# Kernel optimization log

Measured on AMD Instinct MI355X. Metric: run time of the kernel, lower is better.

The kernel has to match this reference:

```python
import jax, jax.numpy as jnp
import numpy as np

V, D, H, L, B = 30000, 128, 4, 128, 512
HD = D // H  # head dim = 32
NL = 2       # num xLSTM layers


def _layernorm(x, w, b):
    mu = x.mean(-1, keepdims=True)
    var = x.var(-1, keepdims=True)
    return (x - mu) * jax.lax.rsqrt(var + 1e-5) * w + b


def _groupnorm_heads(h, w):
    # GroupNorm with num_groups = H over the channel dim (per-head norm), h: [B,L,D]
    hh = h.reshape(h.shape[0], h.shape[1], H, HD)
    mu = hh.mean(-1, keepdims=True)
    var = hh.var(-1, keepdims=True)
    hh = (hh - mu) * jax.lax.rsqrt(var + 1e-5)
    return hh.reshape(h.shape) * w


def _slstm_block(x, W, R, b, gnw, lnw, lnb):
    # x: [B,L,D]; W: [4,D,D] input gate projections (i,f,z,o); R: [4,H,HD,HD] block-diagonal
    # per-head recurrent weights; b: [4,D]; gnw: [D] groupnorm scale.
    bsz = x.shape[0]
    xn = _layernorm(x, lnw, lnb)
    pre = jnp.einsum('bld,god->lbgo', xn, W) + b  # [L,B,4,D]

    def step(carry, pre_t):
        h, c, n, m = carry  # each [B,D]
        rec = jnp.einsum('bhd,ghde->bghe', h.reshape(bsz, H, HD), R).reshape(bsz, 4, D)
        g = pre_t + rec
        it, ft, zt, ot = g[:, 0], g[:, 1], g[:, 2], g[:, 3]
        # stabilized exponential gating (sLSTM vanilla backend)
        m_new = jnp.maximum(ft + m, it)
        i = jnp.exp(it - m_new)
        f = jnp.exp(ft + m - m_new)
        c_new = f * c + i * jnp.tanh(zt)
        n_new = f * n + i
        h_new = jax.nn.sigmoid(ot) * c_new / n_new
        return (h_new, c_new, n_new, m_new), h_new

    z = jnp.zeros((bsz, D), x.dtype)
    _, hs = jax.lax.scan(step, (z, z, z, z), pre)
    hs = jnp.transpose(hs, (1, 0, 2))  # [B,L,D]
    return x + _groupnorm_heads(hs, gnw)  # residual block


def setup_inputs() -> dict:
    key = jax.random.key(0)
    ks = jax.random.split(key, 10)
    s = lambda k, shape, sc: jax.random.normal(k, shape, jnp.float32) * sc
    return {
        'x_ids': jax.random.randint(ks[0], (B, L), 0, V),
        'emb': s(ks[1], (V, D), 0.02),
        'ln_w': jnp.ones((NL, D), jnp.float32),
        'ln_b': jnp.zeros((NL, D), jnp.float32),
        'Wg': s(ks[2], (NL, 4, D, D), 0.05),
        'Rg': s(ks[3], (NL, 4, H, HD, HD), 0.05),
        'bg': s(ks[4], (NL, 4, D), 0.02),
        'gn_w': jnp.ones((NL, D), jnp.float32),
        'w1': s(ks[5], (64, D), 0.05),
        'b1': jnp.zeros((64,), jnp.float32),
        'w2': s(ks[6], (2, 64), 0.05),
        'b2': jnp.zeros((2,), jnp.float32),
    }


def reference(x_ids, emb, ln_w, ln_b, Wg, Rg, bg, gn_w, w1, b1, w2, b2):
    x = emb[x_ids]  # [B,L,D] embedding lookup
    for l in range(NL):
        x = _slstm_block(x, Wg[l], Rg[l], bg[l], gn_w[l], ln_w[l], ln_b[l])
    pooled = x.mean(axis=1)  # mean over sequence, [B,D]
    hid = jax.nn.relu(pooled @ w1.T + b1)  # dropout is identity at eval
    return hid @ w2.T + b2  # [B,2] logits
```

## Files before the change

### kernel.cpp

```cpp
#include <hip/hip_runtime.h>

typedef _Float16 f16;
typedef unsigned int uint;
typedef f16 f16x2 __attribute__((ext_vector_type(2)));
typedef f16 f16x8 __attribute__((ext_vector_type(8)));
typedef __fp16 h16x2 __attribute__((ext_vector_type(2)));
typedef float f32x4 __attribute__((ext_vector_type(4)));

#define Bn 512
#define Ln 128
#define Dn 128
#define Cn 512

__device__ __forceinline__ float fdot2f(uint a, uint b, float c) {
#if __has_builtin(__builtin_amdgcn_fdot2)
  return __builtin_amdgcn_fdot2(__builtin_bit_cast(f16x2, a),
                                __builtin_bit_cast(f16x2, b), c, false);
#else
  f16x2 av = __builtin_bit_cast(f16x2, a), bv = __builtin_bit_cast(f16x2, b);
  return c + (float)av[0] * (float)bv[0] + (float)av[1] * (float)bv[1];
#endif
}

__device__ __forceinline__ uint pk2(float a, float b) {
#if __has_builtin(__builtin_amdgcn_cvt_pkrtz)
  h16x2 v = __builtin_amdgcn_cvt_pkrtz(a, b);
  return __builtin_bit_cast(uint, v);
#else
  f16x2 v; v[0] = (f16)a; v[1] = (f16)b;
  return __builtin_bit_cast(uint, v);
#endif
}

template<int CTRL>
__device__ __forceinline__ float rorf(float x) {
#if __has_builtin(__builtin_amdgcn_mov_dpp)
  int r = __builtin_amdgcn_mov_dpp(__builtin_bit_cast(int, x), CTRL, 0xF, 0xF, true);
  return __builtin_bit_cast(float, r);
#else
  return __shfl_xor(x, (CTRL - 0x120));
#endif
}

__device__ __forceinline__ int swz16i(float x) {
#if __has_builtin(__builtin_amdgcn_ds_swizzle)
  return __builtin_amdgcn_ds_swizzle(__builtin_bit_cast(int, x), 0x401F);
#else
  return __builtin_bit_cast(int, __shfl_xor(x, 16));
#endif
}

__device__ __forceinline__ void read_hu(const f16* base, uint hu[16]) {
  const uint4* hq = (const uint4*)base;
  uint4 q0 = hq[0], q1 = hq[1], q2 = hq[2], q3 = hq[3];
  hu[0]=q0.x; hu[1]=q0.y; hu[2]=q0.z; hu[3]=q0.w;
  hu[4]=q1.x; hu[5]=q1.y; hu[6]=q1.z; hu[7]=q1.w;
  hu[8]=q2.x; hu[9]=q2.y; hu[10]=q2.z; hu[11]=q2.w;
  hu[12]=q3.x; hu[13]=q3.y; hu[14]=q3.z; hu[15]=q3.w;
}

__global__ __launch_bounds__(256) void k_embed_ln(const int* __restrict__ ids,
                                                  const float* __restrict__ emb,
                                                  const float* __restrict__ lw,
                                                  const float* __restrict__ lb,
                                                  float* __restrict__ x,
                                                  f16* __restrict__ xn) {
  int row = blockIdx.x * 4 + (threadIdx.x >> 6);
  int lane = threadIdx.x & 63;
  int id = ids[row];
  const float* er = emb + (size_t)id * Dn;
  float a = er[lane], b = er[lane + 64];
  float s1 = a + b, s2 = a * a + b * b;
  #pragma unroll
  for (int off = 32; off; off >>= 1) {
    s1 += __shfl_xor(s1, off);
    s2 += __shfl_xor(s2, off);
  }
  float mu = s1 * (1.f / 128.f);
  float var = s2 * (1.f / 128.f) - mu * mu;
  float rs = rsqrtf(var + 1e-5f);
  float* xr = x + (size_t)row * Dn;
  xr[lane] = a; xr[lane + 64] = b;
  f16* xo = xn + (size_t)row * Dn;
  xo[lane]      = (f16)((a - mu) * rs * lw[lane] + lb[lane]);
  xo[lane + 64] = (f16)((b - mu) * rs * lw[lane + 64] + lb[lane + 64]);
}

__global__ __launch_bounds__(256) void k_convert(const float* __restrict__ Wg,
                                                 const float* __restrict__ Rg,
                                                 f16* __restrict__ WhF,
                                                 f16* __restrict__ RT) {
  int i = blockIdx.x * 256 + threadIdx.x;
  const int nWfrag = 2 * 4 * 32 * 64;
  if (i < nWfrag) {
    int lane = i & 63;
    int ii   = (i >> 6) & 31;
    int kk   = (i >> 11) & 3;
    int l    = i >> 13;
    int c = ii * 16 + (lane & 15);
    int d = kk * 32 + ((lane >> 4) << 3);
    const float* src = Wg + ((size_t)(l * 512 + c) * 128 + d);
    f16* dst = WhF + (size_t)i * 8;
    #pragma unroll
    for (int j = 0; j < 8; ++j) dst[j] = (f16)src[j];
  } else {
    int j = i - nWfrag;
    if (j < 32768) {
      int dd = j & 31;
      int e  = (j >> 5) & 31;
      int hh = (j >> 10) & 3;
      int g  = (j >> 12) & 3;
      int l  = j >> 14;
      RT[j] = (f16)Rg[((((l * 4 + g) * 4 + hh) * 32 + dd) * 32) + e];
    }
  }
}

__global__ __launch_bounds__(256) void k_ln(const float* __restrict__ x,
                                            const float* __restrict__ lw,
                                            const float* __restrict__ lb,
                                            f16* __restrict__ xn) {
  int row = blockIdx.x * 4 + (threadIdx.x >> 6);
  int lane = threadIdx.x & 63;
  const float* xr = x + (size_t)row * Dn;
  float a = xr[lane], b = xr[lane + 64];
  float s1 = a + b, s2 = a * a + b * b;
  #pragma unroll
  for (int off = 32; off; off >>= 1) {
    s1 += __shfl_xor(s1, off);
    s2 += __shfl_xor(s2, off);
  }
  float mu = s1 * (1.f / 128.f);
  float var = s2 * (1.f / 128.f) - mu * mu;
  float rs = rsqrtf(var + 1e-5f);
  f16* xo = xn + (size_t)row * Dn;
  xo[lane]      = (f16)((a - mu) * rs * lw[lane] + lb[lane]);
  xo[lane + 64] = (f16)((b - mu) * rs * lw[lane + 64] + lb[lane + 64]);
}

__global__ __launch_bounds__(256) void k_gemm(const f16* __restrict__ xn,
                                              const f16* __restrict__ WhF,
                                              const float* __restrict__ bias,
                                              uint2* __restrict__ preP) {
  int w = threadIdx.x >> 6;
  int lane = threadIdx.x & 63;
  int l16 = lane & 15, quad = lane >> 4;
  int m0 = blockIdx.x * 64 + w * 16;

  float bv[32];
  #pragma unroll
  for (int i = 0; i < 32; ++i) bv[i] = bias[i * 16 + l16];

  f16x8 a[4];
  const f16* arow = xn + (size_t)(m0 + l16) * Dn + quad * 8;
  #pragma unroll
  for (int kk = 0; kk < 4; ++kk) a[kk] = *(const f16x8*)(arow + kk * 32);

  f32x4 acc[32] = {};
  const f16* bbase = WhF + (size_t)lane * 8;
  #pragma unroll
  for (int kk = 0; kk < 4; ++kk) {
    #pragma unroll
    for (int i = 0; i < 32; ++i) {
      f16x8 bf = *(const f16x8*)(bbase + (size_t)(kk * 32 + i) * 512);
      acc[i] = __builtin_amdgcn_mfma_f32_16x16x32_f16(a[kk], bf, acc[i], 0, 0, 0);
    }
  }
  #pragma unroll
  for (int r = 0; r < 4; ++r) {
    int m = m0 + quad * 4 + r;
    #pragma unroll
    for (int i7 = 0; i7 < 8; ++i7) {
      uint2 v;
      v.x = pk2(acc[i7][r]      + bv[i7],      acc[i7 + 8][r]  + bv[i7 + 8]);
      v.y = pk2(acc[i7 + 16][r] + bv[i7 + 16], acc[i7 + 24][r] + bv[i7 + 24]);
      preP[(size_t)m * Dn + i7 * 16 + l16] = v;
    }
  }
}

template<int LAST>
__global__ __launch_bounds__(256, 1) void k_scan(const uint2* __restrict__ preP,
                                                 const f16* __restrict__ RT,
                                                 const float* __restrict__ gnw,
                                                 const float* __restrict__ xin,
                                                 float* __restrict__ xout,
                                                 float* __restrict__ pooled) {
  const int w = threadIdx.x >> 6;
  const int lane = threadIdx.x & 63;
  const int s = w >> 1;
  const int b = blockIdx.x * 2 + s;
  const int d = ((w & 1) << 6) + lane;
  const int head = d >> 5;
  const int e = d & 31;
  const int half = lane >> 5;

  __shared__ __align__(16) f16 hsh[4][64];

  uint rr[4][16];
  const uint* RT32 = (const uint*)RT;
  #pragma unroll
  for (int g = 0; g < 4; ++g) {
    const uint* p = RT32 + ((g * 4 + head) * 32 + e) * 16;
    #pragma unroll
    for (int j = 0; j < 16; ++j) rr[g][j] = p[j];
  }
  const float gw = gnw[d];
  const f16* hbase = &hsh[w][half * 32];

  hsh[w][lane] = (f16)0.f;

  const uint2* pp = preP + (size_t)b * Ln * Dn + d;
  const float* xp = xin + (size_t)b * Ln * Dn + d;
  float* xo = xout + (size_t)b * Ln * Dn + d;

  uint2 pb[4]; float xb[4];
  #pragma unroll
  for (int k = 0; k < 4; ++k) { pb[k] = pp[(size_t)k * Dn]; xb[k] = xp[(size_t)k * Dn]; }

  uint hu[16];
  read_hu(hbase, hu);

  float cc = 0.f, nc = 0.f, mc = 0.f, psum = 0.f;
  float hprev = 0.f, xprev = 0.f;
  float u1 = 0.f, u2 = 0.f;
  int   w1 = 0,   w2 = 0;

  #pragma unroll 1
  for (int t = 0; t < Ln; t += 4) {
    #pragma unroll
    for (int k = 0; k < 4; ++k) {
      int tt = t + k;
      uint2 pc = pb[k]; float xc = xb[k];
      pb[k] = pp[(size_t)(tt + 4) * Dn];
      xb[k] = xp[(size_t)(tt + 4) * Dn];

      if (tt > 0) {
        float s1 = u1 + __builtin_bit_cast(float, w1);
        float s2 = u2 + __builtin_bit_cast(float, w2);
        float mu = s1 * (1.f / 32.f);
        float va = s2 * (1.f / 32.f) - mu * mu;
        float ov = xprev + (hprev - mu) * rsqrtf(va + 1e-5f) * gw;
        if (LAST) psum += ov;
        else      xo[(size_t)(tt - 1) * Dn] = ov;
      }

      float a0 = 0.f, a1 = 0.f, a2 = 0.f, a3 = 0.f;
      float c0 = 0.f, c1 = 0.f, c2 = 0.f, c3 = 0.f;
      #pragma unroll
      for (int j = 0; j < 8; ++j) {
        a0 = fdot2f(hu[j], rr[0][j], a0);
        a1 = fdot2f(hu[j], rr[1][j], a1);
        a2 = fdot2f(hu[j], rr[2][j], a2);
        a3 = fdot2f(hu[j], rr[3][j], a3);
        c0 = fdot2f(hu[j + 8], rr[0][j + 8], c0);
        c1 = fdot2f(hu[j + 8], rr[1][j + 8], c1);
        c2 = fdot2f(hu[j + 8], rr[2][j + 8], c2);
        c3 = fdot2f(hu[j + 8], rr[3][j + 8], c3);
      }
      f16x2 lo = __builtin_bit_cast(f16x2, pc.x);
      f16x2 hi = __builtin_bit_cast(f16x2, pc.y);
      float it = ((float)lo[0] + a0) + c0;
      float ft = ((float)lo[1] + a1) + c1;
      float zt = ((float)hi[0] + a2) + c2;
      float ot = ((float)hi[1] + a3) + c3;

      float mn = fmaxf(ft + mc, it);
      float iv = __expf(it - mn);
      float fv = __expf(ft + mc - mn);
      float zc = fminf(fmaxf(zt, -15.f), 15.f);
      float ez = __expf(2.f * zc);
      float tz = (ez - 1.f) * __builtin_amdgcn_rcpf(ez + 1.f);
      float cn = fv * cc + iv * tz;
      float nn = fv * nc + iv;
      float hn = cn * __builtin_amdgcn_rcpf((1.f + __expf(-ot)) * nn);
      cc = cn; nc = nn; mc = mn;

      hsh[w][lane] = (f16)hn;

      float t1v = hn, t2v = hn * hn;
      t1v += rorf<0x121>(t1v);  t2v += rorf<0x121>(t2v);
      t1v += rorf<0x122>(t1v);  t2v += rorf<0x122>(t2v);
      t1v += rorf<0x124>(t1v);  t2v += rorf<0x124>(t2v);
      t1v += rorf<0x128>(t1v);  t2v += rorf<0x128>(t2v);
      w1 = swz16i(t1v);
      w2 = swz16i(t2v);
      u1 = t1v; u2 = t2v;

      read_hu(hbase, hu);

      hprev = hn; xprev = xc;
    }
  }

  {
    float s1 = u1 + __builtin_bit_cast(float, w1);
    float s2 = u2 + __builtin_bit_cast(float, w2);
    float mu = s1 * (1.f / 32.f);
    float va = s2 * (1.f / 32.f) - mu * mu;
    float ov = xprev + (hprev - mu) * rsqrtf(va + 1e-5f) * gw;
    if (LAST) {
      psum += ov;
      pooled[b * Dn + d] = psum * (1.f / 128.f);
    } else {
      xo[(size_t)(Ln - 1) * Dn] = ov;
    }
  }
}

__global__ __launch_bounds__(64) void k_head(const float* __restrict__ pooled,
                                             const float* __restrict__ w1,
                                             const float* __restrict__ b1,
                                             const float* __restrict__ w2,
                                             const float* __restrict__ b2,
                                             float* __restrict__ out) {
  int b = blockIdx.x;
  int tid = threadIdx.x;
  __shared__ float pool[128];
  __shared__ float hid[64];
  pool[tid]      = pooled[b * Dn + tid];
  pool[tid + 64] = pooled[b * Dn + tid + 64];
  __syncthreads();
  {
    float a = b1[tid];
    const float* wr = w1 + (size_t)tid * Dn;
    #pragma unroll 4
    for (int dd = 0; dd < Dn; ++dd) a += pool[dd] * wr[dd];
    hid[tid] = fmaxf(a, 0.f);
  }
  __syncthreads();
  if (tid < 2) {
    float a = b2[tid];
    const float* wr = w2 + tid * 64;
    #pragma unroll 4
    for (int j = 0; j < 64; ++j) a += hid[j] * wr[j];
    out[b * 2 + tid] = a;
  }
}

extern "C" void kernel_launch(void* const* d_in, const int* in_sizes, int n_in,
                              void* d_out, int out_size, void* d_ws, size_t ws_size,
                              hipStream_t stream) {
  const int*   ids  = (const int*)d_in[0];
  const float* emb  = (const float*)d_in[1];
  const float* ln_w = (const float*)d_in[2];
  const float* ln_b = (const float*)d_in[3];
  const float* Wg   = (const float*)d_in[4];
  const float* Rg   = (const float*)d_in[5];
  const float* bg   = (const float*)d_in[6];
  const float* gn_w = (const float*)d_in[7];
  const float* w1   = (const float*)d_in[8];
  const float* b1   = (const float*)d_in[9];
  const float* w2   = (const float*)d_in[10];
  const float* b2   = (const float*)d_in[11];
  float* out = (float*)d_out;

  char* ws = (char*)d_ws;
  float* x     = (float*)ws;
  f16*   xn    = (f16*)(ws + 33554432);
  uint2* preP  = (uint2*)(ws + 33554432 + 16777216);
  f16*   WhF   = (f16*)(ws + 117440512);
  f16*   RT    = (f16*)(ws + 117440512 + 262144);
  float* pooled= (float*)(ws + 117440512 + 262144 + 65536);

  k_embed_ln<<<16384, 256, 0, stream>>>(ids, emb, ln_w, ln_b, x, xn);
  k_convert<<<192, 256, 0, stream>>>(Wg, Rg, WhF, RT);

  k_gemm<<<1024, 256, 0, stream>>>(xn, WhF, bg, preP);
  k_scan<0><<<256, 256, 0, stream>>>(preP, RT, gn_w, x, x, nullptr);
  k_ln<<<16384, 256, 0, stream>>>(x, ln_w + Dn, ln_b + Dn, xn);
  k_gemm<<<1024, 256, 0, stream>>>(xn, WhF + 65536, bg + Cn, preP);
  k_scan<1><<<256, 256, 0, stream>>>(preP, RT + 16384, gn_w + Dn, x, nullptr, pooled);

  k_head<<<512, 64, 0, stream>>>(pooled, w1, b1, w2, b2, out);
}
```

Baseline: 266.8 us.

## Fuse embedding gather and layernorm into GEMM, fold head into final scan

Measured after the change: 269.9 us. About the same (+1.2%).

```diff
diff --git a/kernel.cpp b/kernel.cpp
--- a/kernel.cpp
+++ b/kernel.cpp
@@ -57,33 +57,6 @@
   hu[4]=q1.x; hu[5]=q1.y; hu[6]=q1.z; hu[7]=q1.w;
   hu[8]=q2.x; hu[9]=q2.y; hu[10]=q2.z; hu[11]=q2.w;
   hu[12]=q3.x; hu[13]=q3.y; hu[14]=q3.z; hu[15]=q3.w;
-}
-
-__global__ __launch_bounds__(256) void k_embed_ln(const int* __restrict__ ids,
-                                                  const float* __restrict__ emb,
-                                                  const float* __restrict__ lw,
-                                                  const float* __restrict__ lb,
-                                                  float* __restrict__ x,
-                                                  f16* __restrict__ xn) {
-  int row = blockIdx.x * 4 + (threadIdx.x >> 6);
-  int lane = threadIdx.x & 63;
-  int id = ids[row];
-  const float* er = emb + (size_t)id * Dn;
-  float a = er[lane], b = er[lane + 64];
-  float s1 = a + b, s2 = a * a + b * b;
-  #pragma unroll
-  for (int off = 32; off; off >>= 1) {
-    s1 += __shfl_xor(s1, off);
-    s2 += __shfl_xor(s2, off);
-  }
-  float mu = s1 * (1.f / 128.f);
-  float var = s2 * (1.f / 128.f) - mu * mu;
-  float rs = rsqrtf(var + 1e-5f);
-  float* xr = x + (size_t)row * Dn;
-  xr[lane] = a; xr[lane + 64] = b;
-  f16* xo = xn + (size_t)row * Dn;
-  xo[lane]      = (f16)((a - mu) * rs * lw[lane] + lb[lane]);
-  xo[lane + 64] = (f16)((b - mu) * rs * lw[lane + 64] + lb[lane + 64]);
 }
 
 __global__ __launch_bounds__(256) void k_convert(const float* __restrict__ Wg,
@@ -116,29 +89,11 @@
   }
 }
 
-__global__ __launch_bounds__(256) void k_ln(const float* __restrict__ x,
-                                            const float* __restrict__ lw,
-                                            const float* __restrict__ lb,
-                                            f16* __restrict__ xn) {
-  int row = blockIdx.x * 4 + (threadIdx.x >> 6);
-  int lane = threadIdx.x & 63;
-  const float* xr = x + (size_t)row * Dn;
-  float a = xr[lane], b = xr[lane + 64];
-  float s1 = a + b, s2 = a * a + b * b;
-  #pragma unroll
-  for (int off = 32; off; off >>= 1) {
-    s1 += __shfl_xor(s1, off);
-    s2 += __shfl_xor(s2, off);
-  }
-  float mu = s1 * (1.f / 128.f);
-  float var = s2 * (1.f / 128.f) - mu * mu;
-  float rs = rsqrtf(var + 1e-5f);
-  f16* xo = xn + (size_t)row * Dn;
-  xo[lane]      = (f16)((a - mu) * rs * lw[lane] + lb[lane]);
-  xo[lane + 64] = (f16)((b - mu) * rs * lw[lane + 64] + lb[lane + 64]);
-}
-
-__global__ __launch_bounds__(256) void k_gemm(const f16* __restrict__ xn,
+template<int EMB>
+__global__ __launch_bounds__(256) void k_gemm(const float* __restrict__ xsrc,
+                                              const int* __restrict__ ids,
+                                              const float* __restrict__ lw,
+                                              const float* __restrict__ lb,
                                               const f16* __restrict__ WhF,
                                               const float* __restrict__ bias,
                                               uint2* __restrict__ preP) {
@@ -147,14 +102,50 @@
   int l16 = lane & 15, quad = lane >> 4;
   int m0 = blockIdx.x * 64 + w * 16;
 
+  const float* src;
+  if (EMB) src = xsrc + (size_t)ids[m0 + l16] * Dn;
+  else     src = xsrc + (size_t)(m0 + l16) * Dn;
+  const float* sp = src + quad * 8;
+
+  f32x4 v[4][2];
+  #pragma unroll
+  for (int kk = 0; kk < 4; ++kk) {
+    v[kk][0] = *(const f32x4*)(sp + kk * 32);
+    v[kk][1] = *(const f32x4*)(sp + kk * 32 + 4);
+  }
+  float s1 = 0.f, s2 = 0.f;
+  #pragma unroll
+  for (int kk = 0; kk < 4; ++kk)
+    #pragma unroll
+    for (int p = 0; p < 2; ++p)
+      #pragma unroll
+      for (int j = 0; j < 4; ++j) {
+        float vv = v[kk][p][j];
+        s1 += vv; s2 = fmaf(vv, vv, s2);
+      }
+  s1 += __shfl_xor(s1, 16);  s2 += __shfl_xor(s2, 16);
+  s1 += __shfl_xor(s1, 32);  s2 += __shfl_xor(s2, 32);
+  float mu = s1 * (1.f / 128.f);
+  float var = s2 * (1.f / 128.f) - mu * mu;
+  float rs = rsqrtf(var + 1e-5f);
+
+  f16x8 a[4];
+  #pragma unroll
+  for (int kk = 0; kk < 4; ++kk) {
+    #pragma unroll
+    for (int p = 0; p < 2; ++p) {
+      int d0 = kk * 32 + quad * 8 + p * 4;
+      f32x4 lw4 = *(const f32x4*)(lw + d0);
+      f32x4 lb4 = *(const f32x4*)(lb + d0);
+      #pragma unroll
+      for (int j = 0; j < 4; ++j)
+        a[kk][p * 4 + j] = (f16)((v[kk][p][j] - mu) * rs * lw4[j] + lb4[j]);
+    }
+  }
+
   float bv[32];
   #pragma unroll
   for (int i = 0; i < 32; ++i) bv[i] = bias[i * 16 + l16];
-
-  f16x8 a[4];
-  const f16* arow = xn + (size_t)(m0 + l16) * Dn + quad * 8;
-  #pragma unroll
-  for (int kk = 0; kk < 4; ++kk) a[kk] = *(const f16x8*)(arow + kk * 32);
 
   f32x4 acc[32] = {};
   const f16* bbase = WhF + (size_t)lane * 8;
@@ -171,10 +162,10 @@
     int m = m0 + quad * 4 + r;
     #pragma unroll
     for (int i7 = 0; i7 < 8; ++i7) {
-      uint2 v;
-      v.x = pk2(acc[i7][r]      + bv[i7],      acc[i7 + 8][r]  + bv[i7 + 8]);
-      v.y = pk2(acc[i7 + 16][r] + bv[i7 + 16], acc[i7 + 24][r] + bv[i7 + 24]);
-      preP[(size_t)m * Dn + i7 * 16 + l16] = v;
+      uint2 vv;
+      vv.x = pk2(acc[i7][r]      + bv[i7],      acc[i7 + 8][r]  + bv[i7 + 8]);
+      vv.y = pk2(acc[i7 + 16][r] + bv[i7 + 16], acc[i7 + 24][r] + bv[i7 + 24]);
+      preP[(size_t)m * Dn + i7 * 16 + l16] = vv;
     }
   }
 }
@@ -183,9 +174,14 @@
 __global__ __launch_bounds__(256, 1) void k_scan(const uint2* __restrict__ preP,
                                                  const f16* __restrict__ RT,
                                                  const float* __restrict__ gnw,
-                                                 const float* __restrict__ xin,
+                                                 const float* __restrict__ xsrc,
+                                                 const int* __restrict__ ids,
                                                  float* __restrict__ xout,
-                                                 float* __restrict__ pooled) {
+                                                 const float* __restrict__ hw1,
+                                                 const float* __restrict__ hb1,
+                                                 const float* __restrict__ hw2,
+                                                 const float* __restrict__ hb2,
+                                                 float* __restrict__ out) {
   const int w = threadIdx.x >> 6;
   const int lane = threadIdx.x & 63;
   const int s = w >> 1;
@@ -196,6 +192,8 @@
   const int half = lane >> 5;
 
   __shared__ __align__(16) f16 hsh[4][64];
+  __shared__ float pool2[2][128];
+  __shared__ float hid2[2][64];
 
   uint rr[4][16];
   const uint* RT32 = (const uint*)RT;
@@ -211,12 +209,21 @@
   hsh[w][lane] = (f16)0.f;
 
   const uint2* pp = preP + (size_t)b * Ln * Dn + d;
-  const float* xp = xin + (size_t)b * Ln * Dn + d;
+  const float* xp = xsrc + (size_t)b * Ln * Dn + d;
+  const int*   idr = ids + b * Ln;
   float* xo = xout + (size_t)b * Ln * Dn + d;
 
-  uint2 pb[4]; float xb[4];
-  #pragma unroll
-  for (int k = 0; k < 4; ++k) { pb[k] = pp[(size_t)k * Dn]; xb[k] = xp[(size_t)k * Dn]; }
+  uint2 pb[4]; float xb[4]; int idb[4];
+  #pragma unroll
+  for (int k = 0; k < 4; ++k) {
+    pb[k] = pp[(size_t)k * Dn];
+    if (LAST) {
+      xb[k] = xp[(size_t)k * Dn];
+    } else {
+      xb[k] = xsrc[(size_t)idr[k] * Dn + d];
+      idb[k] = idr[k + 4];
+    }
+  }
 
   uint hu[16];
   read_hu(hbase, hu);
@@ -233,7 +240,13 @@
       int tt = t + k;
       uint2 pc = pb[k]; float xc = xb[k];
       pb[k] = pp[(size_t)(tt + 4) * Dn];
-      xb[k] = xp[(size_t)(tt + 4) * Dn];
+      if (LAST) {
+        xb[k] = xp[(size_t)(tt + 4) * Dn];
+      } else {
+        xb[k] = xsrc[(size_t)idb[k] * Dn + d];
+        int ni = tt + 8;
+        idb[k] = idr[ni > 127 ? 127 : ni];
+      }
 
       if (tt > 0) {
         float s1 = u1 + __builtin_bit_cast(float, w1);
@@ -301,40 +314,32 @@
     float ov = xprev + (hprev - mu) * rsqrtf(va + 1e-5f) * gw;
     if (LAST) {
       psum += ov;
-      pooled[b * Dn + d] = psum * (1.f / 128.f);
+      pool2[s][d] = psum * (1.f / 128.f);
+      __syncthreads();
+      if ((w & 1) == 0) {
+        int sq = w >> 1;
+        float acc = hb1[lane];
+        const float* wr = hw1 + (size_t)lane * Dn;
+        const float* pl = &pool2[sq][0];
+        #pragma unroll 8
+        for (int dd = 0; dd < Dn; dd += 4) {
+          f32x4 wv = *(const f32x4*)(wr + dd);
+          acc += wv[0]*pl[dd] + wv[1]*pl[dd+1] + wv[2]*pl[dd+2] + wv[3]*pl[dd+3];
+        }
+        hid2[sq][lane] = fmaxf(acc, 0.f);
+      }
+      __syncthreads();
+      if ((w & 1) == 0 && lane < 2) {
+        int sq = w >> 1;
+        float acc = hb2[lane];
+        const float* wr = hw2 + lane * 64;
+        #pragma unroll 4
+        for (int j = 0; j < 64; ++j) acc += hid2[sq][j] * wr[j];
+        out[(blockIdx.x * 2 + sq) * 2 + lane] = acc;
+      }
     } else {
       xo[(size_t)(Ln - 1) * Dn] = ov;
     }
-  }
-}
-
-__global__ __launch_bounds__(64) void k_head(const float* __restrict__ pooled,
-                                             const float* __restrict__ w1,
-                                             const float* __restrict__ b1,
-                                             const float* __restrict__ w2,
-                                             const float* __restrict__ b2,
-                                             float* __restrict__ out) {
-  int b = blockIdx.x;
-  int tid = threadIdx.x;
-  __shared__ float pool[128];
-  __shared__ float hid[64];
-  pool[tid]      = pooled[b * Dn + tid];
-  pool[tid + 64] = pooled[b * Dn + tid + 64];
-  __syncthreads();
-  {
-    float a = b1[tid];
-    const float* wr = w1 + (size_t)tid * Dn;
-    #pragma unroll 4
-    for (int dd = 0; dd < Dn; ++dd) a += pool[dd] * wr[dd];
-    hid[tid] = fmaxf(a, 0.f);
-  }
-  __syncthreads();
-  if (tid < 2) {
-    float a = b2[tid];
-    const float* wr = w2 + tid * 64;
-    #pragma unroll 4
-    for (int j = 0; j < 64; ++j) a += hid[j] * wr[j];
-    out[b * 2 + tid] = a;
   }
 }
 
@@ -356,21 +361,18 @@
   float* out = (float*)d_out;
 
   char* ws = (char*)d_ws;
-  float* x     = (float*)ws;
-  f16*   xn    = (f16*)(ws + 33554432);
-  uint2* preP  = (uint2*)(ws + 33554432 + 16777216);
-  f16*   WhF   = (f16*)(ws + 117440512);
-  f16*   RT    = (f16*)(ws + 117440512 + 262144);
-  float* pooled= (float*)(ws + 117440512 + 262144 + 65536);
-
-  k_embed_ln<<<16384, 256, 0, stream>>>(ids, emb, ln_w, ln_b, x, xn);
+  uint2* preP = (uint2*)ws;
+  float* x1   = (float*)(ws + 67108864);
+  f16*   WhF  = (f16*)(ws + 100663296);
+  f16*   RT   = (f16*)(ws + 100663296 + 262144);
+
   k_convert<<<192, 256, 0, stream>>>(Wg, Rg, WhF, RT);
 
-  k_gemm<<<1024, 256, 0, stream>>>(xn, WhF, bg, preP);
-  k_scan<0><<<256, 256, 0, stream>>>(preP, RT, gn_w, x, x, nullptr);
-  k_ln<<<16384, 256, 0, stream>>>(x, ln_w + Dn, ln_b + Dn, xn);
-  k_gemm<<<1024, 256, 0, stream>>>(xn, WhF + 65536, bg + Cn, preP);
-  k_scan<1><<<256, 256, 0, stream>>>(preP, RT + 16384, gn_w + Dn, x, nullptr, pooled);
-
-  k_head<<<512, 64, 0, stream>>>(pooled, w1, b1, w2, b2, out);
-}
+  k_gemm<1><<<1024, 256, 0, stream>>>(emb, ids, ln_w, ln_b, WhF, bg, preP);
+  k_scan<0><<<256, 256, 0, stream>>>(preP, RT, gn_w, emb, ids, x1,
+                                     nullptr, nullptr, nullptr, nullptr, nullptr);
+  k_gemm<0><<<1024, 256, 0, stream>>>(x1, nullptr, ln_w + Dn, ln_b + Dn,
+                                      WhF + 65536, bg + Cn, preP);
+  k_scan<1><<<256, 256, 0, stream>>>(preP, RT + 16384, gn_w + Dn, x1, nullptr,
+                                     nullptr, w1, b1, w2, b2, out);
+}
```
